# Kernel optimization log

Hardware: AMD Instinct MI355X
Metric: run time of the kernel (lower is better)

## Reference

```python
import jax, jax.numpy as jnp
import numpy as np


def setup_inputs() -> dict:
    key = jax.random.key(0)
    k1, k2, k3, k4 = jax.random.split(key, 4)
    B, T, E, H = 16, 2048, 1024, 128
    x = jax.random.normal(k1, (B, T, E), dtype=jnp.float32)
    Wk = jax.random.normal(k2, (E, H), dtype=jnp.float32) * (E ** -0.5)
    Wq = jax.random.normal(k3, (E, H), dtype=jnp.float32) * (E ** -0.5)
    Wv = jax.random.normal(k4, (E, H), dtype=jnp.float32) * (E ** -0.5)
    return {"x": x, "Wk": Wk, "Wq": Wq, "Wv": Wv}


def reference(x, Wk, Wq, Wv):
    # x: [B,T,E]; Wk/Wq/Wv: [E,H]
    B, T, E = x.shape
    H = Wk.shape[1]
    k = jnp.einsum('bte,eh->bth', x, Wk)
    q = jnp.einsum('bte,eh->bth', x, Wq)
    v = jnp.einsum('bte,eh->bth', x, Wv)
    # scores [B,T,T]; original masks with -inf THEN scales (equivalent math)
    scores = jnp.einsum('bqh,bkh->bqk', q, k) * (H ** -0.5)
    causal = jnp.tril(jnp.ones((T, T), dtype=bool))
    scores = jnp.where(causal, scores, -jnp.inf)
    weights = jax.nn.softmax(scores, axis=-1)
    # dropout disabled (eval mode reference)
    return jnp.einsum('bqk,bkh->bqh', weights, v)
```

## Files before the change

### kernel.cpp

```cpp
#include <hip/hip_runtime.h>

#define B_ 16
#define T_ 2048
#define E_ 1024
#define H_ 128

typedef short bf16x8 __attribute__((ext_vector_type(8)));
typedef float f32x4 __attribute__((ext_vector_type(4)));
typedef unsigned short u16x4 __attribute__((ext_vector_type(4)));

static __device__ __forceinline__ unsigned short f2bf(float f) {
    unsigned int u = __float_as_uint(f);
    u += 0x7FFFu + ((u >> 16) & 1u);
    return (unsigned short)(u >> 16);
}
static __device__ __forceinline__ unsigned int pk2(unsigned short a, unsigned short b) {
    return (unsigned int)a | ((unsigned int)b << 16);
}
static __device__ __forceinline__ bf16x8 frag(uint4 v) {
    return __builtin_bit_cast(bf16x8, v);
}

__global__ __launch_bounds__(256) void xcvt_kernel(
    const float* __restrict__ x, unsigned short* __restrict__ xb)
{
    size_t i = ((size_t)blockIdx.x * 256 + threadIdx.x) * 8;
    float4 a = *(const float4*)(x + i);
    float4 b = *(const float4*)(x + i + 4);
    uint4 o;
    o.x = pk2(f2bf(a.x), f2bf(a.y));
    o.y = pk2(f2bf(a.z), f2bf(a.w));
    o.z = pk2(f2bf(b.x), f2bf(b.y));
    o.w = pk2(f2bf(b.z), f2bf(b.w));
    *(uint4*)(xb + i) = o;
}

__global__ __launch_bounds__(256) void wcvt_kernel(
    const float* __restrict__ w0, const float* __restrict__ w1,
    const float* __restrict__ w2, unsigned short* __restrict__ wt)
{
    int g   = blockIdx.x * 256 + threadIdx.x;
    int arr = g >> 14;
    int rem = g & 16383;
    int h   = rem >> 7;
    int e0  = (rem & 127) * 8;
    const float* src = (arr == 0) ? w0 : (arr == 1) ? w1 : w2;
    unsigned short b[8];
#pragma unroll
    for (int i = 0; i < 8; i++) b[i] = f2bf(src[(size_t)(e0 + i) * H_ + h]);
    uint4 o;
    o.x = pk2(b[0], b[1]); o.y = pk2(b[2], b[3]);
    o.z = pk2(b[4], b[5]); o.w = pk2(b[6], b[7]);
    *(uint4*)&wt[(size_t)(arr * 128 + h) * E_ + e0] = o;
}

__global__ __launch_bounds__(256, 2) void proj_kernel(
    const unsigned short* __restrict__ xb,
    const unsigned short* __restrict__ wt,
    unsigned short* __restrict__ q_ws,
    unsigned short* __restrict__ k_ws,
    unsigned short* __restrict__ vt_ws)
{
    const int m0 = blockIdx.x * 128;
    const int by = blockIdx.y;
    __shared__ __align__(16) unsigned short As[128 * 32];
    __shared__ __align__(16) unsigned short Bs[128 * 32];

    const int tid  = threadIdx.x;
    const int lane = tid & 63;
    const int w    = tid >> 6;
    const int quad = lane >> 4;
    const int lm   = lane & 15;
    const int rw   = (w & 1) * 64;
    const int cw   = (w >> 1) * 64;

    const int r0 = tid >> 2;
    const int kc = (tid & 3) * 8;
    const unsigned short* xrow = xb + (size_t)(m0 + r0) * E_ + kc;
    const unsigned short* wrow = wt + (size_t)(by * 128 + r0) * E_ + kc;

    const f32x4 z4 = {0.f, 0.f, 0.f, 0.f};
    f32x4 acc[4][4];
#pragma unroll
    for (int i = 0; i < 4; i++)
#pragma unroll
        for (int j = 0; j < 4; j++) acc[i][j] = z4;

    uint4 pa0 = *(const uint4*)(xrow);
    uint4 pa1 = *(const uint4*)(xrow + (size_t)64 * E_);
    uint4 pb0 = *(const uint4*)(wrow);
    uint4 pb1 = *(const uint4*)(wrow + (size_t)64 * E_);

    for (int kb = 0; kb < 32; kb++) {
        __syncthreads();
        *(uint4*)&As[tid * 8]          = pa0;
        *(uint4*)&As[(tid + 256) * 8]  = pa1;
        *(uint4*)&Bs[tid * 8]          = pb0;
        *(uint4*)&Bs[(tid + 256) * 8]  = pb1;
        __syncthreads();

        const int kn = (kb < 31) ? (kb + 1) * 32 : 0;
        pa0 = *(const uint4*)(xrow + kn);
        pa1 = *(const uint4*)(xrow + (size_t)64 * E_ + kn);
        pb0 = *(const uint4*)(wrow + kn);
        pb1 = *(const uint4*)(wrow + (size_t)64 * E_ + kn);

        bf16x8 a[4], b[4];
#pragma unroll
        for (int am = 0; am < 4; am++)
            a[am] = frag(*(const uint4*)&As[(rw + am * 16 + lm) * 32 + quad * 8]);
#pragma unroll
        for (int bn = 0; bn < 4; bn++)
            b[bn] = frag(*(const uint4*)&Bs[(cw + bn * 16 + lm) * 32 + quad * 8]);
#pragma unroll
        for (int am = 0; am < 4; am++)
#pragma unroll
            for (int bn = 0; bn < 4; bn++)
                acc[am][bn] = __builtin_amdgcn_mfma_f32_16x16x32_bf16(
                    a[am], b[bn], acc[am][bn], 0, 0, 0);
    }

    const int bb = m0 >> 11;
    const int t0 = m0 & 2047;
#pragma unroll
    for (int am = 0; am < 4; am++)
#pragma unroll
        for (int bn = 0; bn < 4; bn++) {
            const int col = cw + bn * 16 + lm;
            const int row = m0 + rw + am * 16 + quad * 4;
            if (by == 0) {
#pragma unroll
                for (int r = 0; r < 4; r++)
                    q_ws[(size_t)(row + r) * H_ + col] = f2bf(acc[am][bn][r]);
            } else if (by == 1) {
#pragma unroll
                for (int r = 0; r < 4; r++)
                    k_ws[(size_t)(row + r) * H_ + col] = f2bf(acc[am][bn][r]);
            } else {
                const int tt = t0 + rw + am * 16 + quad * 4;
                u16x4 p;
#pragma unroll
                for (int r = 0; r < 4; r++) p[r] = f2bf(acc[am][bn][r]);
                *(u16x4*)&vt_ws[((size_t)(bb * 64 + (tt >> 5)) * 128 + col) * 32 + (tt & 31)] = p;
            }
        }
}

__global__ __launch_bounds__(256, 3) void attn_kernel(
    const unsigned short* __restrict__ q_ws,
    const unsigned short* __restrict__ k_ws,
    const unsigned short* __restrict__ vt_ws,
    float* __restrict__ out)
{
    const int batch = blockIdx.x & 15;
    const int pair  = blockIdx.x >> 4;

    __shared__ __align__(16) unsigned short Ps[4][16][40];
    __shared__ __align__(16) float Cb[3][64][40];

    const int tid  = threadIdx.x;
    const int lane = tid & 63;
    const int ww   = tid >> 6;
    const int quad = lane >> 4;
    const int lm   = lane & 15;
    const float scale = 0.08838834764831845f;

    const size_t bq = (size_t)batch * T_ * H_;

    bf16x8 ones;
#pragma unroll
    for (int i = 0; i < 8; i++) ones[i] = (short)0x3F80;

    const f32x4 z4 = {0.f, 0.f, 0.f, 0.f};

    for (int half = 0; half < 2; half++) {
        const int t   = half ? (127 - pair) : pair;
        const int nkt = (t + 2) >> 1;

        bf16x8 qf[4];
#pragma unroll
        for (int h = 0; h < 4; h++)
            qf[h] = frag(*(const uint4*)(q_ws + bq +
                     (size_t)(t * 16 + lm) * H_ + h * 32 + quad * 8));

        f32x4 o[9];
#pragma unroll
        for (int f = 0; f < 9; f++) o[f] = z4;

        for (int kt = ww; kt < nkt; kt += 4) {
            const int k0 = kt * 32;

            uint4 kr[2][4];
#pragma unroll
            for (int hf = 0; hf < 2; hf++)
#pragma unroll
                for (int h = 0; h < 4; h++)
                    kr[hf][h] = *(const uint4*)(k_ws + bq +
                        (size_t)(k0 + hf * 16 + lm) * H_ + h * 32 + quad * 8);

            f32x4 st0 = z4, st1 = z4;
#pragma unroll
            for (int h = 0; h < 4; h++) {
                st0 = __builtin_amdgcn_mfma_f32_16x16x32_bf16(frag(kr[0][h]), qf[h], st0, 0, 0, 0);
                st1 = __builtin_amdgcn_mfma_f32_16x16x32_bf16(frag(kr[1][h]), qf[h], st1, 0, 0, 0);
            }

            uint4 vr[8];
#pragma unroll
            for (int f = 0; f < 8; f++)
                vr[f] = *(const uint4*)(vt_ws +
                    ((size_t)(batch * 64 + kt) * 128 + f * 16 + lm) * 32 + quad * 8);

            const int qg = t * 16 + lm;
            u16x4 pa, pb;
#pragma unroll
            for (int r = 0; r < 4; r++) {
                int kv0 = k0 + quad * 4 + r;
                float e0 = __expf(st0[r] * scale);
                float e1 = __expf(st1[r] * scale);
                pa[r] = (kv0      <= qg) ? f2bf(e0) : (unsigned short)0;
                pb[r] = (kv0 + 16 <= qg) ? f2bf(e1) : (unsigned short)0;
            }
            *(u16x4*)&Ps[ww][lm][quad * 4]      = pa;
            *(u16x4*)&Ps[ww][lm][16 + quad * 4] = pb;
            bf16x8 pf = frag(*(const uint4*)&Ps[ww][lm][quad * 8]);

#pragma unroll
            for (int f = 0; f < 8; f++)
                o[f] = __builtin_amdgcn_mfma_f32_16x16x32_bf16(pf, frag(vr[f]), o[f], 0, 0, 0);
            o[8] = __builtin_amdgcn_mfma_f32_16x16x32_bf16(pf, ones, o[8], 0, 0, 0);
        }

        __syncthreads();
        if (ww) {
#pragma unroll
            for (int f = 0; f < 9; f++) *(f32x4*)&Cb[ww - 1][lane][f * 4] = o[f];
        }
        __syncthreads();
        if (!ww) {
#pragma unroll
            for (int s = 0; s < 3; s++)
#pragma unroll
                for (int f = 0; f < 9; f++)
                    o[f] += *(const f32x4*)&Cb[s][lane][f * 4];
            float* op = out + bq + (size_t)(t * 16) * H_;
#pragma unroll
            for (int r = 0; r < 4; r++) {
                float inv = 1.f / o[8][r];
#pragma unroll
                for (int f = 0; f < 8; f++)
                    op[(size_t)(quad * 4 + r) * H_ + f * 16 + lm] = o[f][r] * inv;
            }
        }
        __syncthreads();
    }
}

extern "C" void kernel_launch(void* const* d_in, const int* in_sizes, int n_in,
                              void* d_out, int out_size, void* d_ws, size_t ws_size,
                              hipStream_t stream)
{
    const float* x  = (const float*)d_in[0];
    const float* Wk = (const float*)d_in[1];
    const float* Wq = (const float*)d_in[2];
    const float* Wv = (const float*)d_in[3];
    float* out = (float*)d_out;

    const size_t MH = (size_t)B_ * T_ * H_;
    const size_t ME = (size_t)B_ * T_ * E_;
    unsigned short* q_ws  = (unsigned short*)d_ws;
    unsigned short* k_ws  = q_ws + MH;
    unsigned short* vt_ws = k_ws + MH;
    unsigned short* wt    = vt_ws + MH;
    unsigned short* xb    = wt + (size_t)384 * E_;

    xcvt_kernel<<<dim3(ME / 2048), dim3(256), 0, stream>>>(x, xb);
    wcvt_kernel<<<dim3(192), dim3(256), 0, stream>>>(Wq, Wk, Wv, wt);
    proj_kernel<<<dim3(256, 3), dim3(256), 0, stream>>>(xb, wt, q_ws, k_ws, vt_ws);
    attn_kernel<<<dim3(1024), dim3(256), 0, stream>>>(q_ws, k_ws, vt_ws, out);
}
```

Measured before the change: 336.3 us.

## Share K/V tiles in LDS across 64-query blocks with dynamic task queue

The attention kernel now gives each block 64 query rows, 16 per wave, instead of splitting one 16-row tile's keys across waves. K and V tiles are staged once per block into LDS via global_load_lds and reused by all four waves, which removes redundant global loads and the cross-wave reduction. Work is handed out through an atomic counter in largest-first order to balance the causal triangle. K is stored in a tiled layout to make the LDS copy contiguous, and the projection GEMM also switches to direct global-to-LDS loads with a higher occupancy bound. The cost is more barriers per key tile and loads that are no longer prefetched ahead of compute.

```diff
diff --git a/kernel.cpp b/kernel.cpp
--- a/kernel.cpp
+++ b/kernel.cpp
@@ -19,6 +19,11 @@
 }
 static __device__ __forceinline__ bf16x8 frag(uint4 v) {
     return __builtin_bit_cast(bf16x8, v);
+}
+static __device__ __forceinline__ void gl16(const unsigned short* g, unsigned short* l) {
+    __builtin_amdgcn_global_load_lds(
+        (const __attribute__((address_space(1))) void*)g,
+        (__attribute__((address_space(3))) void*)l, 16, 0, 0);
 }
 
 __global__ __launch_bounds__(256) void xcvt_kernel(
@@ -54,11 +59,11 @@
     *(uint4*)&wt[(size_t)(arr * 128 + h) * E_ + e0] = o;
 }
 
-__global__ __launch_bounds__(256, 2) void proj_kernel(
+__global__ __launch_bounds__(256, 3) void proj_kernel(
     const unsigned short* __restrict__ xb,
     const unsigned short* __restrict__ wt,
     unsigned short* __restrict__ q_ws,
-    unsigned short* __restrict__ k_ws,
+    unsigned short* __restrict__ kp_ws,
     unsigned short* __restrict__ vt_ws)
 {
     const int m0 = blockIdx.x * 128;
@@ -74,10 +79,16 @@
     const int rw   = (w & 1) * 64;
     const int cw   = (w >> 1) * 64;
 
-    const int r0 = tid >> 2;
-    const int kc = (tid & 3) * 8;
-    const unsigned short* xrow = xb + (size_t)(m0 + r0) * E_ + kc;
-    const unsigned short* wrow = wt + (size_t)(by * 128 + r0) * E_ + kc;
+    const int srow = w * 32 + (lane >> 2);
+    const int sch  = (lane & 3) * 8;
+    const unsigned short* ga0 = xb + (size_t)(m0 + srow) * E_ + sch;
+    const unsigned short* ga1 = ga0 + (size_t)16 * E_;
+    const unsigned short* gb0 = wt + (size_t)(by * 128 + srow) * E_ + sch;
+    const unsigned short* gb1 = gb0 + (size_t)16 * E_;
+    unsigned short* la0 = As + (size_t)(w * 2)     * 512;
+    unsigned short* la1 = As + (size_t)(w * 2 + 1) * 512;
+    unsigned short* lb0 = Bs + (size_t)(w * 2)     * 512;
+    unsigned short* lb1 = Bs + (size_t)(w * 2 + 1) * 512;
 
     const f32x4 z4 = {0.f, 0.f, 0.f, 0.f};
     f32x4 acc[4][4];
@@ -86,24 +97,12 @@
 #pragma unroll
         for (int j = 0; j < 4; j++) acc[i][j] = z4;
 
-    uint4 pa0 = *(const uint4*)(xrow);
-    uint4 pa1 = *(const uint4*)(xrow + (size_t)64 * E_);
-    uint4 pb0 = *(const uint4*)(wrow);
-    uint4 pb1 = *(const uint4*)(wrow + (size_t)64 * E_);
-
     for (int kb = 0; kb < 32; kb++) {
         __syncthreads();
-        *(uint4*)&As[tid * 8]          = pa0;
-        *(uint4*)&As[(tid + 256) * 8]  = pa1;
-        *(uint4*)&Bs[tid * 8]          = pb0;
-        *(uint4*)&Bs[(tid + 256) * 8]  = pb1;
-        __syncthreads();
-
-        const int kn = (kb < 31) ? (kb + 1) * 32 : 0;
-        pa0 = *(const uint4*)(xrow + kn);
-        pa1 = *(const uint4*)(xrow + (size_t)64 * E_ + kn);
-        pb0 = *(const uint4*)(wrow + kn);
-        pb1 = *(const uint4*)(wrow + (size_t)64 * E_ + kn);
+        gl16(ga0, la0); gl16(ga1, la1);
+        gl16(gb0, lb0); gl16(gb1, lb1);
+        __syncthreads();
+        ga0 += 32; ga1 += 32; gb0 += 32; gb1 += 32;
 
         bf16x8 a[4], b[4];
 #pragma unroll
@@ -127,15 +126,20 @@
 #pragma unroll
         for (int bn = 0; bn < 4; bn++) {
             const int col = cw + bn * 16 + lm;
-            const int row = m0 + rw + am * 16 + quad * 4;
             if (by == 0) {
+                const int row = m0 + rw + am * 16 + quad * 4;
 #pragma unroll
                 for (int r = 0; r < 4; r++)
                     q_ws[(size_t)(row + r) * H_ + col] = f2bf(acc[am][bn][r]);
             } else if (by == 1) {
-#pragma unroll
-                for (int r = 0; r < 4; r++)
-                    k_ws[(size_t)(row + r) * H_ + col] = f2bf(acc[am][bn][r]);
+                const int tl = t0 + rw + am * 16 + quad * 4;
+#pragma unroll
+                for (int r = 0; r < 4; r++) {
+                    int t = tl + r;
+                    kp_ws[(size_t)(bb * 64 + (t >> 5)) * 4096 +
+                          (col >> 5) * 1024 + (t & 31) * 32 + (col & 31)] =
+                        f2bf(acc[am][bn][r]);
+                }
             } else {
                 const int tt = t0 + rw + am * 16 + quad * 4;
                 u16x4 p;
@@ -146,17 +150,17 @@
         }
 }
 
-__global__ __launch_bounds__(256, 3) void attn_kernel(
+__global__ __launch_bounds__(256, 4) void attn_kernel(
     const unsigned short* __restrict__ q_ws,
-    const unsigned short* __restrict__ k_ws,
+    const unsigned short* __restrict__ kp_ws,
     const unsigned short* __restrict__ vt_ws,
-    float* __restrict__ out)
-{
-    const int batch = blockIdx.x & 15;
-    const int pair  = blockIdx.x >> 4;
-
+    float* __restrict__ out,
+    int* __restrict__ ctr)
+{
+    __shared__ __align__(16) unsigned short Ks[4096];
+    __shared__ __align__(16) unsigned short Vs[4096];
     __shared__ __align__(16) unsigned short Ps[4][16][40];
-    __shared__ __align__(16) float Cb[3][64][40];
+    __shared__ int s_task;
 
     const int tid  = threadIdx.x;
     const int lane = tid & 63;
@@ -165,53 +169,59 @@
     const int lm   = lane & 15;
     const float scale = 0.08838834764831845f;
 
-    const size_t bq = (size_t)batch * T_ * H_;
-
     bf16x8 ones;
 #pragma unroll
     for (int i = 0; i < 8; i++) ones[i] = (short)0x3F80;
-
     const f32x4 z4 = {0.f, 0.f, 0.f, 0.f};
 
-    for (int half = 0; half < 2; half++) {
-        const int t   = half ? (127 - pair) : pair;
-        const int nkt = (t + 2) >> 1;
+    const int so = ww * 1024 + lane * 8;
+    unsigned short* lk0 = Ks + ww * 1024;
+    unsigned short* lk1 = Ks + ww * 1024 + 512;
+    unsigned short* lv0 = Vs + ww * 1024;
+    unsigned short* lv1 = Vs + ww * 1024 + 512;
+
+    for (;;) {
+        __syncthreads();
+        if (tid == 0) s_task = atomicAdd(ctr, 1);
+        __syncthreads();
+        const int s = s_task;
+        if (s >= 512) break;
+        const int tau   = 31 - (s >> 4);
+        const int batch = s & 15;
+        const size_t bq = (size_t)batch * T_ * H_;
+        const unsigned short* Kt = kp_ws + (size_t)(batch * 64) * 4096 + so;
+        const unsigned short* Vt = vt_ws + (size_t)(batch * 64) * 4096 + so;
 
         bf16x8 qf[4];
 #pragma unroll
         for (int h = 0; h < 4; h++)
             qf[h] = frag(*(const uint4*)(q_ws + bq +
-                     (size_t)(t * 16 + lm) * H_ + h * 32 + quad * 8));
+                     (size_t)(tau * 64 + ww * 16 + lm) * H_ + h * 32 + quad * 8));
 
         f32x4 o[9];
 #pragma unroll
         for (int f = 0; f < 9; f++) o[f] = z4;
 
-        for (int kt = ww; kt < nkt; kt += 4) {
+        const int nkt = 2 * tau + 2;
+        for (int kt = 0; kt < nkt; kt++) {
+            __syncthreads();
+            const unsigned short* kg = Kt + (size_t)kt * 4096;
+            const unsigned short* vg = Vt + (size_t)kt * 4096;
+            gl16(kg, lk0); gl16(kg + 512, lk1);
+            gl16(vg, lv0); gl16(vg + 512, lv1);
+            __syncthreads();
+
+            f32x4 st0 = z4, st1 = z4;
+#pragma unroll
+            for (int h = 0; h < 4; h++) {
+                bf16x8 kf0 = frag(*(const uint4*)&Ks[(h * 32 + lm) * 32 + quad * 8]);
+                bf16x8 kf1 = frag(*(const uint4*)&Ks[(h * 32 + 16 + lm) * 32 + quad * 8]);
+                st0 = __builtin_amdgcn_mfma_f32_16x16x32_bf16(kf0, qf[h], st0, 0, 0, 0);
+                st1 = __builtin_amdgcn_mfma_f32_16x16x32_bf16(kf1, qf[h], st1, 0, 0, 0);
+            }
+
+            const int qg = tau * 64 + ww * 16 + lm;
             const int k0 = kt * 32;
-
-            uint4 kr[2][4];
-#pragma unroll
-            for (int hf = 0; hf < 2; hf++)
-#pragma unroll
-                for (int h = 0; h < 4; h++)
-                    kr[hf][h] = *(const uint4*)(k_ws + bq +
-                        (size_t)(k0 + hf * 16 + lm) * H_ + h * 32 + quad * 8);
-
-            f32x4 st0 = z4, st1 = z4;
-#pragma unroll
-            for (int h = 0; h < 4; h++) {
-                st0 = __builtin_amdgcn_mfma_f32_16x16x32_bf16(frag(kr[0][h]), qf[h], st0, 0, 0, 0);
-                st1 = __builtin_amdgcn_mfma_f32_16x16x32_bf16(frag(kr[1][h]), qf[h], st1, 0, 0, 0);
-            }
-
-            uint4 vr[8];
-#pragma unroll
-            for (int f = 0; f < 8; f++)
-                vr[f] = *(const uint4*)(vt_ws +
-                    ((size_t)(batch * 64 + kt) * 128 + f * 16 + lm) * 32 + quad * 8);
-
-            const int qg = t * 16 + lm;
             u16x4 pa, pb;
 #pragma unroll
             for (int r = 0; r < 4; r++) {
@@ -226,33 +236,21 @@
             bf16x8 pf = frag(*(const uint4*)&Ps[ww][lm][quad * 8]);
 
 #pragma unroll
-            for (int f = 0; f < 8; f++)
-                o[f] = __builtin_amdgcn_mfma_f32_16x16x32_bf16(pf, frag(vr[f]), o[f], 0, 0, 0);
+            for (int f = 0; f < 8; f++) {
+                bf16x8 vfr = frag(*(const uint4*)&Vs[(f * 16 + lm) * 32 + quad * 8]);
+                o[f] = __builtin_amdgcn_mfma_f32_16x16x32_bf16(pf, vfr, o[f], 0, 0, 0);
+            }
             o[8] = __builtin_amdgcn_mfma_f32_16x16x32_bf16(pf, ones, o[8], 0, 0, 0);
         }
 
-        __syncthreads();
-        if (ww) {
-#pragma unroll
-            for (int f = 0; f < 9; f++) *(f32x4*)&Cb[ww - 1][lane][f * 4] = o[f];
+        float* op = out + bq + (size_t)(tau * 64 + ww * 16) * H_;
+#pragma unroll
+        for (int r = 0; r < 4; r++) {
+            float inv = 1.f / o[8][r];
+#pragma unroll
+            for (int f = 0; f < 8; f++)
+                op[(size_t)(quad * 4 + r) * H_ + f * 16 + lm] = o[f][r] * inv;
         }
-        __syncthreads();
-        if (!ww) {
-#pragma unroll
-            for (int s = 0; s < 3; s++)
-#pragma unroll
-                for (int f = 0; f < 9; f++)
-                    o[f] += *(const f32x4*)&Cb[s][lane][f * 4];
-            float* op = out + bq + (size_t)(t * 16) * H_;
-#pragma unroll
-            for (int r = 0; r < 4; r++) {
-                float inv = 1.f / o[8][r];
-#pragma unroll
-                for (int f = 0; f < 8; f++)
-                    op[(size_t)(quad * 4 + r) * H_ + f * 16 + lm] = o[f][r] * inv;
-            }
-        }
-        __syncthreads();
     }
 }
 
@@ -269,13 +267,15 @@
     const size_t MH = (size_t)B_ * T_ * H_;
     const size_t ME = (size_t)B_ * T_ * E_;
     unsigned short* q_ws  = (unsigned short*)d_ws;
-    unsigned short* k_ws  = q_ws + MH;
-    unsigned short* vt_ws = k_ws + MH;
+    unsigned short* kp_ws = q_ws + MH;
+    unsigned short* vt_ws = kp_ws + MH;
     unsigned short* wt    = vt_ws + MH;
     unsigned short* xb    = wt + (size_t)384 * E_;
-
+    int* ctr = (int*)(xb + ME);
+
+    hipMemsetAsync(ctr, 0, 4, stream);
     xcvt_kernel<<<dim3(ME / 2048), dim3(256), 0, stream>>>(x, xb);
     wcvt_kernel<<<dim3(192), dim3(256), 0, stream>>>(Wq, Wk, Wv, wt);
-    proj_kernel<<<dim3(256, 3), dim3(256), 0, stream>>>(xb, wt, q_ws, k_ws, vt_ws);
-    attn_kernel<<<dim3(1024), dim3(256), 0, stream>>>(q_ws, k_ws, vt_ws, out);
-}
+    proj_kernel<<<dim3(256, 3), dim3(256), 0, stream>>>(xb, wt, q_ws, kp_ws, vt_ws);
+    attn_kernel<<<dim3(256), dim3(256), 0, stream>>>(q_ws, kp_ws, vt_ws, out, ctr);
+}
```

Result: faster. 306.3 us (-8.9%).
